# Kernel optimization log

Measured on AMD Instinct MI355X. Metric: run time of the kernel, lower is better.

The kernel has to match this reference:

```python
import jax, jax.numpy as jnp
import numpy as np


def setup_inputs() -> dict:
    key = jax.random.key(0)
    kq, kk, kv, kl = jax.random.split(key, 4)
    B, Nq, Nk, D, Dv = 16, 2048, 2048, 128, 128
    queries = jax.random.normal(kq, (B, Nq, D), dtype=jnp.float32)
    keys = jax.random.normal(kk, (B, Nk, D), dtype=jnp.float32)
    values = jax.random.normal(kv, (B, Nk, Dv), dtype=jnp.float32)
    valid_lens = jax.random.randint(kl, (B,), 0, 2048, dtype=jnp.int64)
    return {"queries": queries, "keys": keys, "values": values, "valid_lens": valid_lens}


def reference(queries, keys, values, valid_lens):
    # queries: (B, Nq, d), keys: (B, Nk, d), values: (B, Nk, dv), valid_lens: (B,)
    d = queries.shape[-1]
    scores = jnp.einsum('bqd,bkd->bqk', queries, keys) / jnp.sqrt(jnp.asarray(d, queries.dtype))
    # masked_softmax: original sets masked score positions to 1e-8 (NOT -inf) before softmax
    nk = scores.shape[-1]
    mask = jnp.arange(nk)[None, :] < valid_lens[:, None]  # (B, Nk)
    scores = jnp.where(mask[:, None, :], scores, jnp.asarray(1e-8, scores.dtype))
    attn = jax.nn.softmax(scores, axis=-1)
    # dropout rate 0.0 -> identity (eval semantics)
    return jnp.einsum('bqk,bkv->bqv', attn, values)
```

## Files before the change

### kernel.cpp

```cpp
#include <hip/hip_runtime.h>
#include <stdint.h>

#define BATCH 16
#define NQ    2048
#define NK    2048
#define DD    128
#define DVV   128

typedef __bf16 bf16_t;
typedef __bf16 bf16x2 __attribute__((ext_vector_type(2)));
typedef __bf16 bf16x4 __attribute__((ext_vector_type(4)));
typedef __bf16 bf16x8 __attribute__((ext_vector_type(8)));
typedef float  f32x4  __attribute__((ext_vector_type(4)));

#define KB_OFF   ((size_t)0)
#define VT_OFF   ((size_t)8 * 1024 * 1024)
#define SUF_OFF  ((size_t)16 * 1024 * 1024)
#define OP_OFF   (SUF_OFF + 65536)
#define LP_OFF   (OP_OFF + (size_t)512 * 16384 * 4)
#define WS_NEED  (LP_OFF + (size_t)512 * 128 * 4)

__device__ __forceinline__ int load_valid_len(const int* VL, int b) {
  bool looks64 = true;
#pragma unroll
  for (int i = 0; i < 16; ++i) {
    int hi = VL[2 * i + 1];
    unsigned lo = (unsigned)VL[2 * i];
    looks64 = looks64 && (hi == 0) && (lo <= 2048u);
  }
  int L = looks64 ? VL[2 * b] : VL[b];
  return min(max(L, 0), NK);
}

__device__ __forceinline__ void gld16(const void* g, void* l) {
  __builtin_amdgcn_global_load_lds(
      (const __attribute__((address_space(1))) unsigned int*)g,
      (__attribute__((address_space(3))) unsigned int*)l, 16, 0, 0);
}

__device__ __forceinline__ f32x4 mfma16(bf16x8 a, bf16x8 b, f32x4 c) {
  return __builtin_amdgcn_mfma_f32_16x16x32_bf16(a, b, c, 0, 0, 0);
}

__global__ void prep_kernel(const float* __restrict__ K, const float* __restrict__ V,
                            const int* __restrict__ VL,
                            bf16_t* __restrict__ Kb, bf16_t* __restrict__ Vt,
                            float* __restrict__ sufV) {
  __shared__ bf16_t tile[128 * 72];
  const int bid = blockIdx.x;
  const int t = threadIdx.x;
  if (bid < 512) {
    size_t base = ((size_t)bid * 256 + t) * 32;
    const float* src = K + base;
    bf16_t* dst = Kb + base;
#pragma unroll
    for (int i = 0; i < 4; ++i) {
      float4 a = ((const float4*)src)[i * 2];
      float4 c = ((const float4*)src)[i * 2 + 1];
      bf16x8 o;
      o[0] = (bf16_t)a.x; o[1] = (bf16_t)a.y; o[2] = (bf16_t)a.z; o[3] = (bf16_t)a.w;
      o[4] = (bf16_t)c.x; o[5] = (bf16_t)c.y; o[6] = (bf16_t)c.z; o[7] = (bf16_t)c.w;
      ((bf16x8*)dst)[i] = o;
    }
    return;
  }
  int v = bid - 512;
  int b = v & 15, kt = v >> 4;
  int L = load_valid_len(VL, b);
  int m = t & 31;
  int g = t >> 5;
  int r2 = m * 2;
  int k0g = kt * 64 + r2;
  const float* src = V + ((size_t)b * NK + k0g) * DVV;
  float sacc[4][4];
#pragma unroll
  for (int i = 0; i < 4; ++i)
#pragma unroll
    for (int j = 0; j < 4; ++j) sacc[i][j] = 0.f;
  bool a0 = (k0g >= L), a1 = (k0g + 1 >= L);
#pragma unroll
  for (int i = 0; i < 4; ++i) {
    int d4 = g * 4 + i * 32;
    float4 u0 = *(const float4*)(src + d4);
    float4 u1 = *(const float4*)(src + DVV + d4);
    *(bf16x2*)&tile[(d4 + 0) * 72 + r2] = (bf16x2){(bf16_t)u0.x, (bf16_t)u1.x};
    *(bf16x2*)&tile[(d4 + 1) * 72 + r2] = (bf16x2){(bf16_t)u0.y, (bf16_t)u1.y};
    *(bf16x2*)&tile[(d4 + 2) * 72 + r2] = (bf16x2){(bf16_t)u0.z, (bf16_t)u1.z};
    *(bf16x2*)&tile[(d4 + 3) * 72 + r2] = (bf16x2){(bf16_t)u0.w, (bf16_t)u1.w};
    if (a0) { sacc[i][0] += u0.x; sacc[i][1] += u0.y; sacc[i][2] += u0.z; sacc[i][3] += u0.w; }
    if (a1) { sacc[i][0] += u1.x; sacc[i][1] += u1.y; sacc[i][2] += u1.z; sacc[i][3] += u1.w; }
  }
  __syncthreads();
#pragma unroll
  for (int off = 1; off < 32; off <<= 1)
#pragma unroll
    for (int i = 0; i < 4; ++i)
#pragma unroll
      for (int j = 0; j < 4; ++j) sacc[i][j] += __shfl_xor(sacc[i][j], off, 64);
  if (m == 0) {
#pragma unroll
    for (int i = 0; i < 4; ++i)
#pragma unroll
      for (int j = 0; j < 4; ++j)
        atomicAdd(&sufV[b * 128 + g * 4 + i * 32 + j], sacc[i][j]);
  }
  int dv = t >> 1, half = t & 1;
  bf16_t* dst = Vt + (size_t)b * DVV * NK + (size_t)dv * NK + kt * 64 + half * 32;
  const bf16_t* srow = &tile[dv * 72 + half * 32];
#pragma unroll
  for (int j = 0; j < 4; ++j)
    *(bf16x8*)(dst + j * 8) = *(const bf16x8*)(srow + j * 8);
}

__launch_bounds__(256, 2)
__global__ void attn_kernel(const float* __restrict__ Q, const bf16_t* __restrict__ Kb,
                            const bf16_t* __restrict__ Vt, const int* __restrict__ VL,
                            float* __restrict__ Opart, float* __restrict__ lpart) {
  __shared__ __align__(16) bf16_t sK[2][64 * 128];
  __shared__ __align__(16) bf16_t sVt[2][128 * 64];
  __shared__ __align__(16) bf16_t sP[4][32 * 64];

  const int bid = blockIdx.x;
  const int tid = threadIdx.x;

  int Ls[16], idxs[16];
#pragma unroll
  for (int i = 0; i < 16; ++i) { Ls[i] = load_valid_len(VL, i); idxs[i] = i; }
  for (int i = 1; i < 16; ++i) {
    int lv = Ls[i], iv = idxs[i], j = i - 1;
    while (j >= 0 && Ls[j] < lv) { Ls[j + 1] = Ls[j]; idxs[j + 1] = idxs[j]; --j; }
    Ls[j + 1] = lv; idxs[j + 1] = iv;
  }
  const int r_  = (bid < 256) ? bid : (767 - bid);
  const int b   = idxs[r_ >> 5];
  const int L   = Ls[r_ >> 5];
  const int sub = r_ & 31;
  const int qt2 = sub >> 1;
  const int s   = sub & 1;
  const int ktiles = (L + 63) >> 6;
  const int t0 = (s * ktiles) >> 1;
  const int t1 = ((s + 1) * ktiles) >> 1;
  const int slot = (b * 16 + qt2) * 2 + s;

  const int wave = tid >> 6;
  const int lane = tid & 63;
  const int col = lane & 15;
  const int quad = lane >> 4;

  bf16x8 qf[2][4];
  {
    const float sc = 0.1275174307f;
#pragma unroll
    for (int m = 0; m < 2; ++m) {
      const float* qrow = Q + ((size_t)b * NQ + qt2 * 128 + wave * 32 + m * 16 + col) * DD + quad * 8;
#pragma unroll
      for (int ks = 0; ks < 4; ++ks) {
        float4 u0 = *(const float4*)(qrow + ks * 32);
        float4 u1 = *(const float4*)(qrow + ks * 32 + 4);
        bf16x8 f;
        f[0] = (bf16_t)(u0.x * sc); f[1] = (bf16_t)(u0.y * sc);
        f[2] = (bf16_t)(u0.z * sc); f[3] = (bf16_t)(u0.w * sc);
        f[4] = (bf16_t)(u1.x * sc); f[5] = (bf16_t)(u1.y * sc);
        f[6] = (bf16_t)(u1.z * sc); f[7] = (bf16_t)(u1.w * sc);
        qf[m][ks] = f;
      }
    }
  }

  const char* Kbyte = (const char*)Kb + (size_t)b * NK * DD * 2;
  const char* Vbyte = (const char*)Vt + (size_t)b * DVV * NK * 2;
  int koff[4], voff[4];
#pragma unroll
  for (int i = 0; i < 4; ++i) {
    int krow = wave * 16 + i * 4 + (lane >> 4);
    koff[i] = krow * 256 + (((lane & 15) ^ (krow & 15)) * 16);
    int vrow = wave * 32 + i * 8 + (lane >> 3);
    voff[i] = vrow * (NK * 2) + (((lane & 7) ^ ((lane >> 3) & 7)) * 16);
  }
  bf16_t* pw = sP[wave];

  f32x4 Oacc[2][8];
#pragma unroll
  for (int m = 0; m < 2; ++m)
#pragma unroll
    for (int o = 0; o < 8; ++o) Oacc[m][o] = (f32x4){0.f, 0.f, 0.f, 0.f};
  float lsum[2][4] = {{0.f, 0.f, 0.f, 0.f}, {0.f, 0.f, 0.f, 0.f}};

  auto issueTile = [&](int kt, int bufi) {
    const char* kb = Kbyte + (size_t)kt * 16384;
    const char* vb = Vbyte + (size_t)kt * 128;
    bf16_t* kl = &sK[bufi][wave * 2048];
    bf16_t* vl = &sVt[bufi][wave * 2048];
#pragma unroll
    for (int i = 0; i < 4; ++i) {
      gld16(kb + koff[i], kl + i * 512);
      gld16(vb + voff[i], vl + i * 512);
    }
  };

  if (t0 < t1) issueTile(t0, 0);
  int bufi = 0;
  for (int kt = t0; kt < t1; ++kt) {
    if (kt + 1 < t1) {
      issueTile(kt + 1, bufi ^ 1);
      asm volatile("s_waitcnt vmcnt(8)\n\ts_barrier" ::: "memory");
    } else {
      asm volatile("s_waitcnt vmcnt(0)\n\ts_barrier" ::: "memory");
    }

    const bf16_t* kb_ = sK[bufi];
    const bf16_t* vb_ = sVt[bufi];

    f32x4 sc4[2][4];
#pragma unroll
    for (int m = 0; m < 2; ++m)
#pragma unroll
      for (int nt = 0; nt < 4; ++nt) sc4[m][nt] = (f32x4){0.f, 0.f, 0.f, 0.f};
#pragma unroll
    for (int ks = 0; ks < 4; ++ks) {
#pragma unroll
      for (int nt = 0; nt < 4; ++nt) {
        bf16x8 bb = *(const bf16x8*)&kb_[(nt * 16 + col) * 128 + (((ks * 4 + quad) ^ col) * 8)];
        sc4[0][nt] = mfma16(qf[0][ks], bb, sc4[0][nt]);
        sc4[1][nt] = mfma16(qf[1][ks], bb, sc4[1][nt]);
      }
    }

    const int key0 = kt * 64;
#pragma unroll
    for (int nt = 0; nt < 4; ++nt) {
      bool valid = (key0 + nt * 16 + col) < L;
#pragma unroll
      for (int m = 0; m < 2; ++m) {
#pragma unroll
        for (int r = 0; r < 4; ++r) {
          float p = __builtin_amdgcn_exp2f(sc4[m][nt][r]);
          p = valid ? p : 0.f;
          lsum[m][r] += p;
          int row = quad * 4 + r;
          int keyc = nt * 16 + col;
          int phys = ((keyc >> 3) ^ (row & 7));
          pw[m * 1024 + row * 64 + phys * 8 + (keyc & 7)] = (bf16_t)p;
        }
      }
    }

#pragma unroll
    for (int ks2 = 0; ks2 < 2; ++ks2) {
      bf16x8 a0 = *(const bf16x8*)&pw[0 * 1024 + col * 64 + (((ks2 * 4 + quad) ^ (col & 7)) * 8)];
      bf16x8 a1 = *(const bf16x8*)&pw[1 * 1024 + col * 64 + (((ks2 * 4 + quad) ^ (col & 7)) * 8)];
#pragma unroll
      for (int o = 0; o < 8; ++o) {
        bf16x8 bb = *(const bf16x8*)&vb_[(o * 16 + col) * 64 + (((ks2 * 4 + quad) ^ (col & 7)) * 8)];
        Oacc[0][o] = mfma16(a0, bb, Oacc[0][o]);
        Oacc[1][o] = mfma16(a1, bb, Oacc[1][o]);
      }
    }
    asm volatile("s_barrier" ::: "memory");
    bufi ^= 1;
  }

#pragma unroll
  for (int off = 1; off < 16; off <<= 1)
#pragma unroll
    for (int m = 0; m < 2; ++m)
#pragma unroll
      for (int r = 0; r < 4; ++r) lsum[m][r] += __shfl_xor(lsum[m][r], off, 64);

  float* Op = Opart + (size_t)slot * 16384;
#pragma unroll
  for (int m = 0; m < 2; ++m) {
    int rowb = wave * 32 + m * 16 + quad * 4;
#pragma unroll
    for (int o = 0; o < 8; ++o)
#pragma unroll
      for (int r = 0; r < 4; ++r)
        Op[(rowb + r) * 128 + o * 16 + col] = Oacc[m][o][r];
    if (col == 0) {
#pragma unroll
      for (int r = 0; r < 4; ++r)
        lpart[slot * 128 + rowb + r] = lsum[m][r];
    }
  }
}

__global__ void combine_kernel(const float* __restrict__ Opart, const float* __restrict__ lpart,
                               const float* __restrict__ sufV, const int* __restrict__ VL,
                               float* __restrict__ Out) {
  int u = blockIdx.x;
  int b = u & 15, qt2 = u >> 4;
  int L = load_valid_len(VL, b);
  int slot0 = (b * 16 + qt2) * 2;
  int t = threadIdx.x;
  int dv = t & 127, rh = t >> 7;
  const float* O0 = Opart + (size_t)slot0 * 16384;
  const float* O1 = O0 + 16384;
  float suf = sufV[b * 128 + dv];
  float wmask = (float)(NK - L);
  float* Ob = Out + ((size_t)b * NQ + qt2 * 128) * DVV;
  for (int r = rh; r < 128; r += 2) {
    float l = lpart[slot0 * 128 + r] + lpart[(slot0 + 1) * 128 + r] + wmask;
    Ob[(size_t)r * 128 + dv] = (O0[r * 128 + dv] + O1[r * 128 + dv] + suf) / l;
  }
}

#define KSTR 152
#define VSTR 88
#define PSTR 72

__global__ void suffix_fb(const float* __restrict__ V, const int* __restrict__ VL,
                          float* __restrict__ ws) {
  int b = blockIdx.x;
  int kc = blockIdx.y;
  int L = load_valid_len(VL, b);
  int k0 = kc * 128, k1 = k0 + 128;
  int lo = max(L, k0);
  int t = threadIdx.x;
  int dv = t & 127;
  int h = t >> 7;
  float s = 0.f;
  for (int k = lo + h; k < k1; k += 2)
    s += V[((size_t)b * NK + k) * DVV + dv];
  __shared__ float part[128];
  if (h == 0) part[dv] = s;
  __syncthreads();
  if (h == 1) atomicAdd(&ws[b * DVV + dv], part[dv] + s);
}

__launch_bounds__(256, 2)
__global__ void attn_fb(const float* __restrict__ Q, const float* __restrict__ K,
                        const float* __restrict__ V, const int* __restrict__ VL,
                        const float* __restrict__ sufV, float* __restrict__ Out) {
  const int flat = blockIdx.x;
  const int b  = flat & 15;
  const int qt = flat >> 4;
  const int L  = load_valid_len(VL, b);

  __shared__ bf16_t sK2[64 * KSTR];
  __shared__ bf16_t sVT2[128 * VSTR];
  __shared__ bf16_t sP2[4 * 16 * PSTR];

  const int tid  = threadIdx.x;
  const int wave = tid >> 6;
  const int lane = tid & 63;
  const int col  = lane & 15;
  const int quad = lane >> 4;

  const float* Qb = Q + ((size_t)b * NQ + qt * 64 + wave * 16) * DD;
  const float* Kb = K + (size_t)b * NK * DD;
  const float* Vb = V + (size_t)b * NK * DVV;

  bf16x8 qf[4];
  {
    const float scq = 0.08838834764831845f;
    const float* qrow = Qb + (size_t)col * DD + quad * 8;
#pragma unroll
    for (int ks = 0; ks < 4; ++ks) {
      float4 u0 = *(const float4*)(qrow + ks * 32);
      float4 u1 = *(const float4*)(qrow + ks * 32 + 4);
      bf16x8 f;
      f[0] = (bf16_t)(u0.x * scq); f[1] = (bf16_t)(u0.y * scq);
      f[2] = (bf16_t)(u0.z * scq); f[3] = (bf16_t)(u0.w * scq);
      f[4] = (bf16_t)(u1.x * scq); f[5] = (bf16_t)(u1.y * scq);
      f[6] = (bf16_t)(u1.z * scq); f[7] = (bf16_t)(u1.w * scq);
      qf[ks] = f;
    }
  }

  f32x4 Oacc[8];
#pragma unroll
  for (int o = 0; o < 8; ++o) Oacc[o] = (f32x4){0.f, 0.f, 0.f, 0.f};
  float m_i[4], l_i[4];
#pragma unroll
  for (int r = 0; r < 4; ++r) { m_i[r] = -1e30f; l_i[r] = 0.f; }

  const int ktiles = (L + 63) >> 6;
  for (int kt = 0; kt < ktiles; ++kt) {
    {
      int r0 = tid >> 5;
      int d4 = (tid & 31) * 4;
      const float* src = Kb + ((size_t)(kt * 64) + r0) * DD + d4;
#pragma unroll
      for (int i = 0; i < 8; ++i) {
        float4 u = *(const float4*)(src + (size_t)i * 8 * DD);
        bf16x4 w4 = {(bf16_t)u.x, (bf16_t)u.y, (bf16_t)u.z, (bf16_t)u.w};
        *(bf16x4*)&sK2[(r0 + i * 8) * KSTR + d4] = w4;
      }
    }
    {
      int r2 = (tid & 31) * 2;
      int dbase = (tid >> 5) * 4;
#pragma unroll
      for (int i = 0; i < 4; ++i) {
        int d4 = dbase + i * 32;
        const float* s0 = Vb + ((size_t)(kt * 64) + r2) * DVV + d4;
        float4 u0 = *(const float4*)s0;
        float4 u1 = *(const float4*)(s0 + DVV);
        *(bf16x2*)&sVT2[(d4 + 0) * VSTR + r2] = (bf16x2){(bf16_t)u0.x, (bf16_t)u1.x};
        *(bf16x2*)&sVT2[(d4 + 1) * VSTR + r2] = (bf16x2){(bf16_t)u0.y, (bf16_t)u1.y};
        *(bf16x2*)&sVT2[(d4 + 2) * VSTR + r2] = (bf16x2){(bf16_t)u0.z, (bf16_t)u1.z};
        *(bf16x2*)&sVT2[(d4 + 3) * VSTR + r2] = (bf16x2){(bf16_t)u0.w, (bf16_t)u1.w};
      }
    }
    __syncthreads();

    f32x4 sv4[4];
#pragma unroll
    for (int nt = 0; nt < 4; ++nt) sv4[nt] = (f32x4){0.f, 0.f, 0.f, 0.f};
#pragma unroll
    for (int ks = 0; ks < 4; ++ks) {
      bf16x8 a = qf[ks];
#pragma unroll
      for (int nt = 0; nt < 4; ++nt) {
        bf16x8 bb = *(const bf16x8*)&sK2[(nt * 16 + col) * KSTR + ks * 32 + quad * 8];
        sv4[nt] = mfma16(a, bb, sv4[nt]);
      }
    }

    const int key0 = kt * 64;
    float sv[4][4];
    float mloc[4] = {-1e30f, -1e30f, -1e30f, -1e30f};
#pragma unroll
    for (int nt = 0; nt < 4; ++nt) {
      int key = key0 + nt * 16 + col;
      bool valid = key < L;
#pragma unroll
      for (int r = 0; r < 4; ++r) {
        float v = valid ? sv4[nt][r] : -1e30f;
        sv[nt][r] = v;
        mloc[r] = fmaxf(mloc[r], v);
      }
    }
#pragma unroll
    for (int off = 1; off < 16; off <<= 1)
#pragma unroll
      for (int r = 0; r < 4; ++r) mloc[r] = fmaxf(mloc[r], __shfl_xor(mloc[r], off, 64));
    float al[4];
#pragma unroll
    for (int r = 0; r < 4; ++r) {
      float mn = fmaxf(m_i[r], mloc[r]);
      al[r] = __expf(m_i[r] - mn);
      m_i[r] = mn;
    }
    float lloc[4] = {0.f, 0.f, 0.f, 0.f};
#pragma unroll
    for (int nt = 0; nt < 4; ++nt)
#pragma unroll
      for (int r = 0; r < 4; ++r) {
        float p = __expf(sv[nt][r] - m_i[r]);
        sv[nt][r] = p;
        lloc[r] += p;
      }
#pragma unroll
    for (int off = 1; off < 16; off <<= 1)
#pragma unroll
      for (int r = 0; r < 4; ++r) lloc[r] += __shfl_xor(lloc[r], off, 64);
#pragma unroll
    for (int r = 0; r < 4; ++r) l_i[r] = l_i[r] * al[r] + lloc[r];
#pragma unroll
    for (int o = 0; o < 8; ++o)
#pragma unroll
      for (int r = 0; r < 4; ++r) Oacc[o][r] *= al[r];

    bf16_t* pw = &sP2[wave * 16 * PSTR];
#pragma unroll
    for (int nt = 0; nt < 4; ++nt)
#pragma unroll
      for (int r = 0; r < 4; ++r)
        pw[(quad * 4 + r) * PSTR + nt * 16 + col] = (bf16_t)sv[nt][r];

#pragma unroll
    for (int ks2 = 0; ks2 < 2; ++ks2) {
      bf16x8 a = *(const bf16x8*)&pw[(lane & 15) * PSTR + ks2 * 32 + quad * 8];
#pragma unroll
      for (int o = 0; o < 8; ++o) {
        bf16x8 bb = *(const bf16x8*)&sVT2[(o * 16 + col) * VSTR + ks2 * 32 + quad * 8];
        Oacc[o] = mfma16(a, bb, Oacc[o]);
      }
    }
    __syncthreads();
  }

  if (L < NK) {
    const float c = 1e-8f;
    const float w = (float)(NK - L);
    float a2[4], ec[4];
#pragma unroll
    for (int r = 0; r < 4; ++r) {
      float mn = fmaxf(m_i[r], c);
      a2[r] = __expf(m_i[r] - mn);
      ec[r] = __expf(c - mn);
      l_i[r] = l_i[r] * a2[r] + w * ec[r];
    }
    const float* sfv = sufV + b * DVV;
#pragma unroll
    for (int o = 0; o < 8; ++o) {
      float svv = sfv[o * 16 + col];
#pragma unroll
      for (int r = 0; r < 4; ++r) Oacc[o][r] = Oacc[o][r] * a2[r] + ec[r] * svv;
    }
  }

  float invl[4];
#pragma unroll
  for (int r = 0; r < 4; ++r) invl[r] = 1.0f / l_i[r];

  float* Ob = Out + ((size_t)b * NQ + qt * 64 + wave * 16) * DVV;
#pragma unroll
  for (int o = 0; o < 8; ++o)
#pragma unroll
    for (int r = 0; r < 4; ++r)
      Ob[(size_t)(quad * 4 + r) * DVV + o * 16 + col] = Oacc[o][r] * invl[r];
}

extern "C" void kernel_launch(void* const* d_in, const int* in_sizes, int n_in,
                              void* d_out, int out_size, void* d_ws, size_t ws_size,
                              hipStream_t stream) {
  const float* Q  = (const float*)d_in[0];
  const float* K  = (const float*)d_in[1];
  const float* V  = (const float*)d_in[2];
  const int*   VL = (const int*)d_in[3];
  float* out = (float*)d_out;

  if (ws_size >= WS_NEED) {
    char* ws = (char*)d_ws;
    bf16_t* Kb = (bf16_t*)(ws + KB_OFF);
    bf16_t* Vt = (bf16_t*)(ws + VT_OFF);
    float* sufV = (float*)(ws + SUF_OFF);
    float* Opart = (float*)(ws + OP_OFF);
    float* lpart = (float*)(ws + LP_OFF);

    hipMemsetAsync(sufV, 0, BATCH * DVV * sizeof(float), stream);
    prep_kernel<<<1024, 256, 0, stream>>>(K, V, VL, Kb, Vt, sufV);
    attn_kernel<<<512, 256, 0, stream>>>(Q, Kb, Vt, VL, Opart, lpart);
    combine_kernel<<<256, 256, 0, stream>>>(Opart, lpart, sufV, VL, out);
  } else {
    float* ws = (float*)d_ws;
    hipMemsetAsync(ws, 0, BATCH * DVV * sizeof(float), stream);
    dim3 g1(BATCH, 16);
    suffix_fb<<<g1, 256, 0, stream>>>(V, VL, ws);
    attn_fb<<<BATCH * (NQ / 64), 256, 0, stream>>>(Q, K, V, VL, ws, out);
  }
}
```

Before: 162.5 us.

## Split attention block across eight waves with sixteen query rows each

The attention kernel now launches 512 threads per block (8 waves), each wave owning 16 query rows instead of 32. Per-thread state (Q fragments, O accumulators, scores) is halved and K/V tile loading is spread across more waves, with the vmcnt wait adjusted to match. The goal is more waves in flight to hide latency, at the cost of reusing each loaded K/V fragment from LDS across fewer rows per wave, so LDS read traffic per MFMA doubles.

Result: slower. 182.1 us (+12.1%).

```diff
diff --git a/kernel.cpp b/kernel.cpp
--- a/kernel.cpp
+++ b/kernel.cpp
@@ -112,13 +112,13 @@
     *(bf16x8*)(dst + j * 8) = *(const bf16x8*)(srow + j * 8);
 }
 
-__launch_bounds__(256, 2)
+__launch_bounds__(512, 4)
 __global__ void attn_kernel(const float* __restrict__ Q, const bf16_t* __restrict__ Kb,
                             const bf16_t* __restrict__ Vt, const int* __restrict__ VL,
                             float* __restrict__ Opart, float* __restrict__ lpart) {
   __shared__ __align__(16) bf16_t sK[2][64 * 128];
   __shared__ __align__(16) bf16_t sVt[2][128 * 64];
-  __shared__ __align__(16) bf16_t sP[4][32 * 64];
+  __shared__ __align__(16) bf16_t sP[8][16 * 64];
 
   const int bid = blockIdx.x;
   const int tid = threadIdx.x;
@@ -147,52 +147,47 @@
   const int col = lane & 15;
   const int quad = lane >> 4;
 
-  bf16x8 qf[2][4];
+  bf16x8 qf[4];
   {
     const float sc = 0.1275174307f;
-#pragma unroll
-    for (int m = 0; m < 2; ++m) {
-      const float* qrow = Q + ((size_t)b * NQ + qt2 * 128 + wave * 32 + m * 16 + col) * DD + quad * 8;
-#pragma unroll
-      for (int ks = 0; ks < 4; ++ks) {
-        float4 u0 = *(const float4*)(qrow + ks * 32);
-        float4 u1 = *(const float4*)(qrow + ks * 32 + 4);
-        bf16x8 f;
-        f[0] = (bf16_t)(u0.x * sc); f[1] = (bf16_t)(u0.y * sc);
-        f[2] = (bf16_t)(u0.z * sc); f[3] = (bf16_t)(u0.w * sc);
-        f[4] = (bf16_t)(u1.x * sc); f[5] = (bf16_t)(u1.y * sc);
-        f[6] = (bf16_t)(u1.z * sc); f[7] = (bf16_t)(u1.w * sc);
-        qf[m][ks] = f;
-      }
+    const float* qrow = Q + ((size_t)b * NQ + qt2 * 128 + wave * 16 + col) * DD + quad * 8;
+#pragma unroll
+    for (int ks = 0; ks < 4; ++ks) {
+      float4 u0 = *(const float4*)(qrow + ks * 32);
+      float4 u1 = *(const float4*)(qrow + ks * 32 + 4);
+      bf16x8 f;
+      f[0] = (bf16_t)(u0.x * sc); f[1] = (bf16_t)(u0.y * sc);
+      f[2] = (bf16_t)(u0.z * sc); f[3] = (bf16_t)(u0.w * sc);
+      f[4] = (bf16_t)(u1.x * sc); f[5] = (bf16_t)(u1.y * sc);
+      f[6] = (bf16_t)(u1.z * sc); f[7] = (bf16_t)(u1.w * sc);
+      qf[ks] = f;
     }
   }
 
   const char* Kbyte = (const char*)Kb + (size_t)b * NK * DD * 2;
   const char* Vbyte = (const char*)Vt + (size_t)b * DVV * NK * 2;
-  int koff[4], voff[4];
-#pragma unroll
-  for (int i = 0; i < 4; ++i) {
-    int krow = wave * 16 + i * 4 + (lane >> 4);
+  int koff[2], voff[2];
+#pragma unroll
+  for (int i = 0; i < 2; ++i) {
+    int krow = wave * 8 + i * 4 + (lane >> 4);
     koff[i] = krow * 256 + (((lane & 15) ^ (krow & 15)) * 16);
-    int vrow = wave * 32 + i * 8 + (lane >> 3);
+    int vrow = wave * 16 + i * 8 + (lane >> 3);
     voff[i] = vrow * (NK * 2) + (((lane & 7) ^ ((lane >> 3) & 7)) * 16);
   }
   bf16_t* pw = sP[wave];
 
-  f32x4 Oacc[2][8];
-#pragma unroll
-  for (int m = 0; m < 2; ++m)
-#pragma unroll
-    for (int o = 0; o < 8; ++o) Oacc[m][o] = (f32x4){0.f, 0.f, 0.f, 0.f};
-  float lsum[2][4] = {{0.f, 0.f, 0.f, 0.f}, {0.f, 0.f, 0.f, 0.f}};
+  f32x4 Oacc[8];
+#pragma unroll
+  for (int o = 0; o < 8; ++o) Oacc[o] = (f32x4){0.f, 0.f, 0.f, 0.f};
+  float lsum[4] = {0.f, 0.f, 0.f, 0.f};
 
   auto issueTile = [&](int kt, int bufi) {
     const char* kb = Kbyte + (size_t)kt * 16384;
     const char* vb = Vbyte + (size_t)kt * 128;
-    bf16_t* kl = &sK[bufi][wave * 2048];
-    bf16_t* vl = &sVt[bufi][wave * 2048];
-#pragma unroll
-    for (int i = 0; i < 4; ++i) {
+    bf16_t* kl = &sK[bufi][wave * 1024];
+    bf16_t* vl = &sVt[bufi][wave * 1024];
+#pragma unroll
+    for (int i = 0; i < 2; ++i) {
       gld16(kb + koff[i], kl + i * 512);
       gld16(vb + voff[i], vl + i * 512);
     }
@@ -203,7 +198,7 @@
   for (int kt = t0; kt < t1; ++kt) {
     if (kt + 1 < t1) {
       issueTile(kt + 1, bufi ^ 1);
-      asm volatile("s_waitcnt vmcnt(8)\n\ts_barrier" ::: "memory");
+      asm volatile("s_waitcnt vmcnt(4)\n\ts_barrier" ::: "memory");
     } else {
       asm volatile("s_waitcnt vmcnt(0)\n\ts_barrier" ::: "memory");
     }
@@ -211,18 +206,16 @@
     const bf16_t* kb_ = sK[bufi];
     const bf16_t* vb_ = sVt[bufi];
 
-    f32x4 sc4[2][4];
-#pragma unroll
-    for (int m = 0; m < 2; ++m)
-#pragma unroll
-      for (int nt = 0; nt < 4; ++nt) sc4[m][nt] = (f32x4){0.f, 0.f, 0.f, 0.f};
+    f32x4 sc4[4];
+#pragma unroll
+    for (int nt = 0; nt < 4; ++nt) sc4[nt] = (f32x4){0.f, 0.f, 0.f, 0.f};
 #pragma unroll
     for (int ks = 0; ks < 4; ++ks) {
+      bf16x8 a = qf[ks];
 #pragma unroll
       for (int nt = 0; nt < 4; ++nt) {
         bf16x8 bb = *(const bf16x8*)&kb_[(nt * 16 + col) * 128 + (((ks * 4 + quad) ^ col) * 8)];
-        sc4[0][nt] = mfma16(qf[0][ks], bb, sc4[0][nt]);
-        sc4[1][nt] = mfma16(qf[1][ks], bb, sc4[1][nt]);
+        sc4[nt] = mfma16(a, bb, sc4[nt]);
       }
     }
 
@@ -231,29 +224,24 @@
     for (int nt = 0; nt < 4; ++nt) {
       bool valid = (key0 + nt * 16 + col) < L;
 #pragma unroll
-      for (int m = 0; m < 2; ++m) {
-#pragma unroll
-        for (int r = 0; r < 4; ++r) {
-          float p = __builtin_amdgcn_exp2f(sc4[m][nt][r]);
-          p = valid ? p : 0.f;
-          lsum[m][r] += p;
-          int row = quad * 4 + r;
-          int keyc = nt * 16 + col;
-          int phys = ((keyc >> 3) ^ (row & 7));
-          pw[m * 1024 + row * 64 + phys * 8 + (keyc & 7)] = (bf16_t)p;
-        }
+      for (int r = 0; r < 4; ++r) {
+        float p = __builtin_amdgcn_exp2f(sc4[nt][r]);
+        p = valid ? p : 0.f;
+        lsum[r] += p;
+        int row = quad * 4 + r;
+        int keyc = nt * 16 + col;
+        int phys = ((keyc >> 3) ^ (row & 7));
+        pw[row * 64 + phys * 8 + (keyc & 7)] = (bf16_t)p;
       }
     }
 
 #pragma unroll
     for (int ks2 = 0; ks2 < 2; ++ks2) {
-      bf16x8 a0 = *(const bf16x8*)&pw[0 * 1024 + col * 64 + (((ks2 * 4 + quad) ^ (col & 7)) * 8)];
-      bf16x8 a1 = *(const bf16x8*)&pw[1 * 1024 + col * 64 + (((ks2 * 4 + quad) ^ (col & 7)) * 8)];
+      bf16x8 a = *(const bf16x8*)&pw[col * 64 + (((ks2 * 4 + quad) ^ (col & 7)) * 8)];
 #pragma unroll
       for (int o = 0; o < 8; ++o) {
         bf16x8 bb = *(const bf16x8*)&vb_[(o * 16 + col) * 64 + (((ks2 * 4 + quad) ^ (col & 7)) * 8)];
-        Oacc[0][o] = mfma16(a0, bb, Oacc[0][o]);
-        Oacc[1][o] = mfma16(a1, bb, Oacc[1][o]);
+        Oacc[o] = mfma16(a, bb, Oacc[o]);
       }
     }
     asm volatile("s_barrier" ::: "memory");
@@ -263,24 +251,19 @@
 #pragma unroll
   for (int off = 1; off < 16; off <<= 1)
 #pragma unroll
-    for (int m = 0; m < 2; ++m)
-#pragma unroll
-      for (int r = 0; r < 4; ++r) lsum[m][r] += __shfl_xor(lsum[m][r], off, 64);
+    for (int r = 0; r < 4; ++r) lsum[r] += __shfl_xor(lsum[r], off, 64);
 
   float* Op = Opart + (size_t)slot * 16384;
-#pragma unroll
-  for (int m = 0; m < 2; ++m) {
-    int rowb = wave * 32 + m * 16 + quad * 4;
-#pragma unroll
-    for (int o = 0; o < 8; ++o)
-#pragma unroll
-      for (int r = 0; r < 4; ++r)
-        Op[(rowb + r) * 128 + o * 16 + col] = Oacc[m][o][r];
-    if (col == 0) {
-#pragma unroll
-      for (int r = 0; r < 4; ++r)
-        lpart[slot * 128 + rowb + r] = lsum[m][r];
-    }
+  const int rowb = wave * 16 + quad * 4;
+#pragma unroll
+  for (int o = 0; o < 8; ++o)
+#pragma unroll
+    for (int r = 0; r < 4; ++r)
+      Op[(rowb + r) * 128 + o * 16 + col] = Oacc[o][r];
+  if (col == 0) {
+#pragma unroll
+    for (int r = 0; r < 4; ++r)
+      lpart[slot * 128 + rowb + r] = lsum[r];
   }
 }
 
@@ -532,7 +515,7 @@
 
     hipMemsetAsync(sufV, 0, BATCH * DVV * sizeof(float), stream);
     prep_kernel<<<1024, 256, 0, stream>>>(K, V, VL, Kb, Vt, sufV);
-    attn_kernel<<<512, 256, 0, stream>>>(Q, Kb, Vt, VL, Opart, lpart);
+    attn_kernel<<<512, 512, 0, stream>>>(Q, Kb, Vt, VL, Opart, lpart);
     combine_kernel<<<256, 256, 0, stream>>>(Opart, lpart, sufV, VL, out);
   } else {
     float* ws = (float*)d_ws;
```
